# Kernel optimization log

Measured on AMD Instinct MI355X. Metric: run time of the kernel, lower is better.

Reference implementation:

```python
import jax, jax.numpy as jnp
import numpy as np

EPS = 1e-7  # Keras K.epsilon()


def setup_inputs() -> dict:
    key = jax.random.key(0)
    ks = jax.random.split(key, 8)
    B, T, D = 64, 2048, 256
    context = jax.random.normal(ks[0], (B, T, D), dtype=jnp.float32)
    aspect = jax.random.normal(ks[1], (B, D), dtype=jnp.float32)
    sentence = jax.random.normal(ks[2], (B, D), dtype=jnp.float32)
    context_mask = jax.random.randint(ks[3], (B, T), 0, 2).astype(bool)
    context_w = jax.random.normal(ks[4], (D, D), dtype=jnp.float32) * 0.05
    aspect_w = jax.random.normal(ks[5], (D, D), dtype=jnp.float32) * 0.05
    sent_w = jax.random.normal(ks[6], (D, D), dtype=jnp.float32) * 0.05
    attend_w = jax.random.normal(ks[7], (D, 1), dtype=jnp.float32) * 0.05
    return {"context": context, "aspect": aspect, "sentence": sentence,
            "context_mask": context_mask, "context_w": context_w,
            "aspect_w": aspect_w, "sent_w": sent_w, "attend_w": attend_w}


def reference(context, aspect, sentence, context_mask, context_w, aspect_w, sent_w, attend_w):
    # bias term from aspect/sentence, broadcast over time instead of K.repeat: [B,1,D]
    bias = (aspect @ aspect_w + sentence @ sent_w)[:, None, :]
    h = jnp.tanh(jnp.einsum('btd,de->bte', context, context_w) + bias)  # [B,T,D]
    g = jnp.einsum('btd,d->bt', h, attend_w[:, 0])                      # [B,T]
    a = jnp.exp(g) * context_mask.astype(jnp.float32)                   # faithful: no max-subtract
    a = a / (jnp.sum(a, axis=-1, keepdims=True) + EPS)
    attend_context = jnp.einsum('btd,bt->bd', context, a) + sentence     # [B,D]
    return attend_context
```

## Files before the change

### kernel.cpp

```cpp
#include <hip/hip_runtime.h>
#include <hip/hip_bf16.h>

#define BB  64
#define TT  2048
#define DD  256
#define EPSV 1e-7f
#define TILE_R 32
#define NTILE  8
#define NBLK   512

typedef __attribute__((ext_vector_type(8))) short bf16x8;
typedef __attribute__((ext_vector_type(4))) float f32x4;

__device__ __forceinline__ ushort f2bf(float f) {
    union { float f; unsigned u; } v; v.f = f;
    unsigned u = v.u;
    unsigned r = (u + 0x7FFFu + ((u >> 16) & 1u)) >> 16;
    return (ushort)r;
}

__device__ __forceinline__ float bf2f(unsigned h16) {
    union { unsigned u; float f; } v; v.u = h16 << 16;
    return v.f;
}

__device__ __forceinline__ unsigned pkbf(float lo, float hi) {
    union { float f; unsigned u; } a, b;
    a.f = lo; b.f = hi;
    return __builtin_amdgcn_perm(b.u + 0x8000u, a.u + 0x8000u, 0x07060302u);
}

__device__ __forceinline__ float tanh_fast(float x) {
    float e = __expf(2.0f * x);
    return 1.0f - 2.0f * __builtin_amdgcn_rcpf(e + 1.0f);
}

template<int CTRL>
__device__ __forceinline__ float dpp_rot_add(float x) {
    union { float f; int i; } a; a.f = x;
    int r = __builtin_amdgcn_update_dpp(0, a.i, CTRL, 0xF, 0xF, true);
    union { int i; float f; } b; b.i = r;
    return x + b.f;
}
__device__ __forceinline__ float row16_sum(float x) {
    x = dpp_rot_add<0x121>(x);
    x = dpp_rot_add<0x122>(x);
    x = dpp_rot_add<0x124>(x);
    x = dpp_rot_add<0x128>(x);
    return x;
}

__global__ __launch_bounds__(256) void prep_kernel(
    const float* __restrict__ aspect, const float* __restrict__ sentence,
    const float* __restrict__ context_w, const float* __restrict__ aspect_w,
    const float* __restrict__ sent_w,
    float* __restrict__ bias_part, ushort* __restrict__ wfrag_ws)
{
    const int blk = blockIdx.x, tid = threadIdx.x;
    if (blk < 512) {
        const int b = blk >> 3, q = blk & 7, e = tid;
        float s = 0.f;
        #pragma unroll 4
        for (int dd = 0; dd < 32; ++dd) {
            const int d = q * 32 + dd;
            s = fmaf(aspect[b * DD + d],   aspect_w[d * DD + e], s);
            s = fmaf(sentence[b * DD + d], sent_w[d * DD + e],   s);
        }
        bias_part[blk * DD + e] = s;
    } else {
        const int flat = (blk - 512) * 256 + tid;
        const int lane = flat & 63;
        const int kn   = flat >> 6;
        const int kk   = kn >> 4;
        const int n    = kn & 15;
        const int krow = kk * 32 + ((lane >> 4) << 3);
        const int col  = n * 16 + (lane & 15);
        bf16x8 v;
        #pragma unroll
        for (int j = 0; j < 8; ++j)
            v[j] = (short)f2bf(context_w[(size_t)(krow + j) * DD + col]);
        *reinterpret_cast<bf16x8*>(wfrag_ws + (size_t)flat * 8) = v;
    }
}

__global__ __launch_bounds__(512, 2) void attn_main(
    const float* __restrict__ ctx, const int* __restrict__ mask,
    const float* __restrict__ attend_w,
    const float* __restrict__ bias_part, const ushort* __restrict__ wfrag_ws,
    float* __restrict__ partial_ws, float* __restrict__ esum_ws)
{
    __shared__ __align__(16) char bfb[3][TILE_R * 512];
    __shared__ float gpartT[2][8][TILE_R];
    __shared__ float bias_lds[256];
    __shared__ float aw_lds[256];
    __shared__ float mask_lds[256];
    __shared__ float part_d[8][256];

    const int tid  = threadIdx.x;
    const int wave = tid >> 6;
    const int lane = tid & 63;
    const int blk  = blockIdx.x;
    const int b    = blk >> 3;
    const int cg   = wave;

    if (tid < 256) {
        float bs = 0.f;
        #pragma unroll
        for (int q = 0; q < 8; ++q) bs += bias_part[(b * 8 + q) * DD + tid];
        bias_lds[tid] = bs;
    } else {
        const int m = tid - 256;
        aw_lds[m]   = attend_w[m];
        mask_lds[m] = (float)mask[blk * 256 + m];
    }

    bf16x8 Bf[8][2];
    {
        const bf16x8* wf = reinterpret_cast<const bf16x8*>(wfrag_ws);
        #pragma unroll
        for (int kk = 0; kk < 8; ++kk) {
            Bf[kk][0] = wf[(kk * 16 + cg * 2 + 0) * 64 + lane];
            Bf[kk][1] = wf[(kk * 16 + cg * 2 + 1) * 64 + lane];
        }
    }

    const float4* src = reinterpret_cast<const float4*>(ctx);
    const int cc  = tid;
    const int crow0 = cc >> 5,        c80 = cc & 31;
    const int crow1 = (512 + cc) >> 5, c81 = (512 + cc) & 31;

    float4 sreg[4];
    {
        const size_t base4 = (size_t)(blk * NTILE) * 2048;
        #pragma unroll
        for (int i = 0; i < 2; ++i) {
            const int c = i * 512 + tid;
            sreg[2 * i + 0] = src[base4 + 2 * c + 0];
            sreg[2 * i + 1] = src[base4 + 2 * c + 1];
        }
        char* dst = bfb[0];
        #pragma unroll
        for (int i = 0; i < 2; ++i) {
            const int row = i ? crow1 : crow0, c8 = i ? c81 : c80;
            uint4 u;
            u.x = pkbf(sreg[2 * i].x,     sreg[2 * i].y);
            u.y = pkbf(sreg[2 * i].z,     sreg[2 * i].w);
            u.z = pkbf(sreg[2 * i + 1].x, sreg[2 * i + 1].y);
            u.w = pkbf(sreg[2 * i + 1].z, sreg[2 * i + 1].w);
            *reinterpret_cast<uint4*>(dst + row * 512 + ((c8 * 16) ^ ((row & 7) << 4))) = u;
        }
        const size_t b1 = base4 + 2048;
        #pragma unroll
        for (int i = 0; i < 2; ++i) {
            const int c = i * 512 + tid;
            sreg[2 * i + 0] = src[b1 + 2 * c + 0];
            sreg[2 * i + 1] = src[b1 + 2 * c + 1];
        }
    }
    __syncthreads();

    const int c0 = cg * 32 + (lane & 15), c1 = c0 + 16;
    const float bs0 = bias_lds[c0], awc0 = aw_lds[c0];
    const float bs1 = bias_lds[c1], awc1 = aw_lds[c1];

    float accd[4] = {0.f, 0.f, 0.f, 0.f};
    float es_acc = 0.f;
    int cb = 0;

    for (int it = 0; it < NTILE; ++it) {
        const int nb = (cb == 2) ? 0 : cb + 1;
        const int gp = it & 1;
        const char* lb = bfb[cb];

        if (it + 1 < NTILE) {
            char* dst = bfb[nb];
            #pragma unroll
            for (int i = 0; i < 2; ++i) {
                const int row = i ? crow1 : crow0, c8 = i ? c81 : c80;
                uint4 u;
                u.x = pkbf(sreg[2 * i].x,     sreg[2 * i].y);
                u.y = pkbf(sreg[2 * i].z,     sreg[2 * i].w);
                u.z = pkbf(sreg[2 * i + 1].x, sreg[2 * i + 1].y);
                u.w = pkbf(sreg[2 * i + 1].z, sreg[2 * i + 1].w);
                *reinterpret_cast<uint4*>(dst + row * 512 + ((c8 * 16) ^ ((row & 7) << 4))) = u;
            }
        }
        if (it + 2 < NTILE) {
            const size_t base4 = (size_t)(blk * NTILE + it + 2) * 2048;
            #pragma unroll
            for (int i = 0; i < 2; ++i) {
                const int c = i * 512 + tid;
                sreg[2 * i + 0] = src[base4 + 2 * c + 0];
                sreg[2 * i + 1] = src[base4 + 2 * c + 1];
            }
        }

        f32x4 acc[2][2];
        #pragma unroll
        for (int rt = 0; rt < 2; ++rt) {
            acc[rt][0] = (f32x4){0.f, 0.f, 0.f, 0.f};
            acc[rt][1] = (f32x4){0.f, 0.f, 0.f, 0.f};
        }
        #pragma unroll
        for (int rt = 0; rt < 2; ++rt) {
            const int row = rt * 16 + (lane & 15);
            const char* ab = lb + row * 512;
            const int asw = (row & 7) << 4;
            #pragma unroll
            for (int kk = 0; kk < 8; ++kk) {
                const bf16x8 a = *reinterpret_cast<const bf16x8*>(
                    ab + ((kk * 64 + ((lane >> 4) << 4)) ^ asw));
                acc[rt][0] = __builtin_amdgcn_mfma_f32_16x16x32_bf16(a, Bf[kk][0], acc[rt][0], 0, 0, 0);
                acc[rt][1] = __builtin_amdgcn_mfma_f32_16x16x32_bf16(a, Bf[kk][1], acc[rt][1], 0, 0, 0);
            }
        }

        #pragma unroll
        for (int rt = 0; rt < 2; ++rt) {
            float g0 = row16_sum(tanh_fast(acc[rt][0][0] + bs0) * awc0
                               + tanh_fast(acc[rt][1][0] + bs1) * awc1);
            float g1 = row16_sum(tanh_fast(acc[rt][0][1] + bs0) * awc0
                               + tanh_fast(acc[rt][1][1] + bs1) * awc1);
            float g2 = row16_sum(tanh_fast(acc[rt][0][2] + bs0) * awc0
                               + tanh_fast(acc[rt][1][2] + bs1) * awc1);
            float g3 = row16_sum(tanh_fast(acc[rt][0][3] + bs0) * awc0
                               + tanh_fast(acc[rt][1][3] + bs1) * awc1);
            if ((lane & 15) == 0) {
                const int r = rt * 16 + ((lane >> 4) << 2);
                *reinterpret_cast<float4*>(&gpartT[gp][cg][r]) = (float4){g0, g1, g2, g3};
            }
        }
        __syncthreads();

        const int erow = lane & 31;
        float gsum = 0.f;
        #pragma unroll
        for (int c = 0; c < 8; ++c) gsum += gpartT[gp][c][erow];
        const float ev = __expf(gsum) * mask_lds[it * TILE_R + erow];
        es_acc += (lane < 32) ? ev : 0.f;

        #pragma unroll
        for (int rr = 0; rr < 4; ++rr) {
            const int r = wave * 4 + rr;
            const float e = __shfl(ev, r);
            const uint2 hv = *reinterpret_cast<const uint2*>(
                lb + r * 512 + ((lane * 8) ^ ((r & 7) << 4)));
            accd[0] = fmaf(bf2f(hv.x & 0xffffu), e, accd[0]);
            accd[1] = fmaf(bf2f(hv.x >> 16),     e, accd[1]);
            accd[2] = fmaf(bf2f(hv.y & 0xffffu), e, accd[2]);
            accd[3] = fmaf(bf2f(hv.y >> 16),     e, accd[3]);
        }

        cb = nb;
    }

    *reinterpret_cast<float4*>(&part_d[wave][lane * 4]) =
        (float4){accd[0], accd[1], accd[2], accd[3]};
    __syncthreads();
    if (tid < 256) {
        float s = 0.f;
        #pragma unroll
        for (int w = 0; w < 8; ++w) s += part_d[w][tid];
        partial_ws[blk * DD + tid] = s;
    }
    if (wave == 0) {
        float s = row16_sum(es_acc);
        s += __shfl_xor(s, 16);
        if (lane == 0) esum_ws[blk] = s;
    }
}

__global__ __launch_bounds__(256) void finalize_kernel(
    const float* __restrict__ sentence, const float* __restrict__ partial_ws,
    const float* __restrict__ esum_ws, float* __restrict__ out)
{
    const int b = blockIdx.x, d = threadIdx.x;
    float es = 0.f, s = 0.f;
    #pragma unroll
    for (int i = 0; i < 8; ++i) {
        es += esum_ws[b * 8 + i];
        s  += partial_ws[(size_t)(b * 8 + i) * DD + d];
    }
    out[b * DD + d] = s / (es + EPSV) + sentence[b * DD + d];
}

extern "C" void kernel_launch(void* const* d_in, const int* in_sizes, int n_in,
                              void* d_out, int out_size, void* d_ws, size_t ws_size,
                              hipStream_t stream)
{
    const float* ctx       = (const float*)d_in[0];
    const float* aspect    = (const float*)d_in[1];
    const float* sentence  = (const float*)d_in[2];
    const int*   mask      = (const int*)  d_in[3];
    const float* context_w = (const float*)d_in[4];
    const float* aspect_w  = (const float*)d_in[5];
    const float* sent_w    = (const float*)d_in[6];
    const float* attend_w  = (const float*)d_in[7];
    float* out = (float*)d_out;

    char* ws = (char*)d_ws;
    ushort* wfrag_ws   = (ushort*)(ws);
    float*  bias_part  = (float*) (ws + 131072);
    float*  esum_ws    = (float*) (ws + 131072 + 524288);
    float*  partial_ws = (float*) (ws + 131072 + 524288 + 2048);

    prep_kernel<<<544, 256, 0, stream>>>(aspect, sentence, context_w, aspect_w, sent_w,
                                         bias_part, wfrag_ws);
    attn_main<<<NBLK, 512, 0, stream>>>(ctx, mask, attend_w, bias_part, wfrag_ws,
                                        partial_ws, esum_ws);
    finalize_kernel<<<BB, 256, 0, stream>>>(sentence, partial_ws, esum_ws, out);
}
```

Baseline: 46.89 us.

## Fuse prep kernel into attention kernel; compute bias and weight fragments in-block

Removes the separate prep launch. Each attention block now converts its own context_w fragments to bf16 straight from global memory and computes the aspect/sentence bias as two half-sums in LDS. The goal is to drop a kernel launch and the workspace round trip, and to overlap the first context tile loads with this setup work. In exchange every block (512 of them) redoes the 256x256x2 bias matvec for its batch and the strided weight conversion, which adds redundant global reads and ALU work. Launch bounds are also raised to 4 blocks per CU, which may constrain registers.

```diff
diff --git a/kernel.cpp b/kernel.cpp
--- a/kernel.cpp
+++ b/kernel.cpp
@@ -50,48 +50,17 @@
     return x;
 }
 
-__global__ __launch_bounds__(256) void prep_kernel(
+__global__ __launch_bounds__(512, 4) void attn_main(
+    const float* __restrict__ ctx, const int* __restrict__ mask,
+    const float* __restrict__ attend_w,
     const float* __restrict__ aspect, const float* __restrict__ sentence,
     const float* __restrict__ context_w, const float* __restrict__ aspect_w,
     const float* __restrict__ sent_w,
-    float* __restrict__ bias_part, ushort* __restrict__ wfrag_ws)
-{
-    const int blk = blockIdx.x, tid = threadIdx.x;
-    if (blk < 512) {
-        const int b = blk >> 3, q = blk & 7, e = tid;
-        float s = 0.f;
-        #pragma unroll 4
-        for (int dd = 0; dd < 32; ++dd) {
-            const int d = q * 32 + dd;
-            s = fmaf(aspect[b * DD + d],   aspect_w[d * DD + e], s);
-            s = fmaf(sentence[b * DD + d], sent_w[d * DD + e],   s);
-        }
-        bias_part[blk * DD + e] = s;
-    } else {
-        const int flat = (blk - 512) * 256 + tid;
-        const int lane = flat & 63;
-        const int kn   = flat >> 6;
-        const int kk   = kn >> 4;
-        const int n    = kn & 15;
-        const int krow = kk * 32 + ((lane >> 4) << 3);
-        const int col  = n * 16 + (lane & 15);
-        bf16x8 v;
-        #pragma unroll
-        for (int j = 0; j < 8; ++j)
-            v[j] = (short)f2bf(context_w[(size_t)(krow + j) * DD + col]);
-        *reinterpret_cast<bf16x8*>(wfrag_ws + (size_t)flat * 8) = v;
-    }
-}
-
-__global__ __launch_bounds__(512, 2) void attn_main(
-    const float* __restrict__ ctx, const int* __restrict__ mask,
-    const float* __restrict__ attend_w,
-    const float* __restrict__ bias_part, const ushort* __restrict__ wfrag_ws,
     float* __restrict__ partial_ws, float* __restrict__ esum_ws)
 {
     __shared__ __align__(16) char bfb[3][TILE_R * 512];
     __shared__ float gpartT[2][8][TILE_R];
-    __shared__ float bias_lds[256];
+    __shared__ float bias_half[2][256];
     __shared__ float aw_lds[256];
     __shared__ float mask_lds[256];
     __shared__ float part_d[8][256];
@@ -102,31 +71,11 @@
     const int blk  = blockIdx.x;
     const int b    = blk >> 3;
     const int cg   = wave;
-
-    if (tid < 256) {
-        float bs = 0.f;
-        #pragma unroll
-        for (int q = 0; q < 8; ++q) bs += bias_part[(b * 8 + q) * DD + tid];
-        bias_lds[tid] = bs;
-    } else {
-        const int m = tid - 256;
-        aw_lds[m]   = attend_w[m];
-        mask_lds[m] = (float)mask[blk * 256 + m];
-    }
-
-    bf16x8 Bf[8][2];
-    {
-        const bf16x8* wf = reinterpret_cast<const bf16x8*>(wfrag_ws);
-        #pragma unroll
-        for (int kk = 0; kk < 8; ++kk) {
-            Bf[kk][0] = wf[(kk * 16 + cg * 2 + 0) * 64 + lane];
-            Bf[kk][1] = wf[(kk * 16 + cg * 2 + 1) * 64 + lane];
-        }
-    }
+    const int l15  = lane & 15, hi = lane >> 4;
 
     const float4* src = reinterpret_cast<const float4*>(ctx);
     const int cc  = tid;
-    const int crow0 = cc >> 5,        c80 = cc & 31;
+    const int crow0 = cc >> 5,         c80 = cc & 31;
     const int crow1 = (512 + cc) >> 5, c81 = (512 + cc) & 31;
 
     float4 sreg[4];
@@ -138,6 +87,44 @@
             sreg[2 * i + 0] = src[base4 + 2 * c + 0];
             sreg[2 * i + 1] = src[base4 + 2 * c + 1];
         }
+    }
+
+    bf16x8 Bf[8][2];
+    #pragma unroll
+    for (int kk = 0; kk < 8; ++kk) {
+        #pragma unroll
+        for (int n2 = 0; n2 < 2; ++n2) {
+            const int col  = (cg * 2 + n2) * 16 + l15;
+            const int krow = kk * 32 + hi * 8;
+            const float* wp = context_w + (size_t)krow * DD + col;
+            bf16x8 v;
+            #pragma unroll
+            for (int j = 0; j < 8; ++j)
+                v[j] = (short)f2bf(wp[j * DD]);
+            Bf[kk][n2] = v;
+        }
+    }
+
+    if (tid < 256) {
+        aw_lds[tid]   = attend_w[tid];
+        mask_lds[tid] = (float)mask[blk * 256 + tid];
+    }
+    {
+        const int e = tid & 255, h = tid >> 8;
+        const float* ap = aspect   + b * DD + h * 128;
+        const float* sp = sentence + b * DD + h * 128;
+        const float* awp = aspect_w + (size_t)(h * 128) * DD + e;
+        const float* swp = sent_w   + (size_t)(h * 128) * DD + e;
+        float bsum = 0.f;
+        #pragma unroll 4
+        for (int dd = 0; dd < 128; ++dd) {
+            bsum = fmaf(ap[dd], awp[(size_t)dd * DD], bsum);
+            bsum = fmaf(sp[dd], swp[(size_t)dd * DD], bsum);
+        }
+        bias_half[h][e] = bsum;
+    }
+
+    {
         char* dst = bfb[0];
         #pragma unroll
         for (int i = 0; i < 2; ++i) {
@@ -149,7 +136,7 @@
             u.w = pkbf(sreg[2 * i + 1].z, sreg[2 * i + 1].w);
             *reinterpret_cast<uint4*>(dst + row * 512 + ((c8 * 16) ^ ((row & 7) << 4))) = u;
         }
-        const size_t b1 = base4 + 2048;
+        const size_t b1 = (size_t)(blk * NTILE + 1) * 2048;
         #pragma unroll
         for (int i = 0; i < 2; ++i) {
             const int c = i * 512 + tid;
@@ -159,9 +146,9 @@
     }
     __syncthreads();
 
-    const int c0 = cg * 32 + (lane & 15), c1 = c0 + 16;
-    const float bs0 = bias_lds[c0], awc0 = aw_lds[c0];
-    const float bs1 = bias_lds[c1], awc1 = aw_lds[c1];
+    const int c0 = cg * 32 + l15, c1 = c0 + 16;
+    const float bs0 = bias_half[0][c0] + bias_half[1][c0], awc0 = aw_lds[c0];
+    const float bs1 = bias_half[0][c1] + bias_half[1][c1], awc1 = aw_lds[c1];
 
     float accd[4] = {0.f, 0.f, 0.f, 0.f};
     float es_acc = 0.f;
@@ -203,13 +190,13 @@
         }
         #pragma unroll
         for (int rt = 0; rt < 2; ++rt) {
-            const int row = rt * 16 + (lane & 15);
+            const int row = rt * 16 + l15;
             const char* ab = lb + row * 512;
             const int asw = (row & 7) << 4;
             #pragma unroll
             for (int kk = 0; kk < 8; ++kk) {
                 const bf16x8 a = *reinterpret_cast<const bf16x8*>(
-                    ab + ((kk * 64 + ((lane >> 4) << 4)) ^ asw));
+                    ab + ((kk * 64 + (hi << 4)) ^ asw));
                 acc[rt][0] = __builtin_amdgcn_mfma_f32_16x16x32_bf16(a, Bf[kk][0], acc[rt][0], 0, 0, 0);
                 acc[rt][1] = __builtin_amdgcn_mfma_f32_16x16x32_bf16(a, Bf[kk][1], acc[rt][1], 0, 0, 0);
             }
@@ -225,8 +212,8 @@
                                + tanh_fast(acc[rt][1][2] + bs1) * awc1);
             float g3 = row16_sum(tanh_fast(acc[rt][0][3] + bs0) * awc0
                                + tanh_fast(acc[rt][1][3] + bs1) * awc1);
-            if ((lane & 15) == 0) {
-                const int r = rt * 16 + ((lane >> 4) << 2);
+            if (l15 == 0) {
+                const int r = rt * 16 + (hi << 2);
                 *reinterpret_cast<float4*>(&gpartT[gp][cg][r]) = (float4){g0, g1, g2, g3};
             }
         }
@@ -299,14 +286,11 @@
     float* out = (float*)d_out;
 
     char* ws = (char*)d_ws;
-    ushort* wfrag_ws   = (ushort*)(ws);
-    float*  bias_part  = (float*) (ws + 131072);
-    float*  esum_ws    = (float*) (ws + 131072 + 524288);
-    float*  partial_ws = (float*) (ws + 131072 + 524288 + 2048);
-
-    prep_kernel<<<544, 256, 0, stream>>>(aspect, sentence, context_w, aspect_w, sent_w,
-                                         bias_part, wfrag_ws);
-    attn_main<<<NBLK, 512, 0, stream>>>(ctx, mask, attend_w, bias_part, wfrag_ws,
+    float* esum_ws    = (float*)(ws);
+    float* partial_ws = (float*)(ws + 2048);
+
+    attn_main<<<NBLK, 512, 0, stream>>>(ctx, mask, attend_w, aspect, sentence,
+                                        context_w, aspect_w, sent_w,
                                         partial_ws, esum_ws);
     finalize_kernel<<<BB, 256, 0, stream>>>(sentence, partial_ws, esum_ws, out);
 }
```

Result: slower. 158.1 us (+237.3%).

## Software-pipeline weighted-sum stage one tile behind MFMA and raise MFMA priority

Applied to the files above, without the earlier changes.

Moves the exp/mask/weighted context accumulation for tile t to the start of iteration t+1, so it runs alongside the next tile's staging and MFMA work instead of right after the barrier. The LDS ring buffer grows from 3 to 4 slots so the previous tile's bf16 data stays valid while it is read. s_setprio is raised around the MFMA loop to favour matrix issue across waves. The extra 16KB of LDS per block may reduce occupancy under the 2-blocks-per-CU launch bound.

```diff
diff --git a/kernel.cpp b/kernel.cpp
--- a/kernel.cpp
+++ b/kernel.cpp
@@ -89,7 +89,7 @@
     const float* __restrict__ bias_part, const ushort* __restrict__ wfrag_ws,
     float* __restrict__ partial_ws, float* __restrict__ esum_ws)
 {
-    __shared__ __align__(16) char bfb[3][TILE_R * 512];
+    __shared__ __align__(16) char bfb[4][TILE_R * 512];
     __shared__ float gpartT[2][8][TILE_R];
     __shared__ float bias_lds[256];
     __shared__ float aw_lds[256];
@@ -102,6 +102,7 @@
     const int blk  = blockIdx.x;
     const int b    = blk >> 3;
     const int cg   = wave;
+    const int l15  = lane & 15, hi = lane >> 4;
 
     if (tid < 256) {
         float bs = 0.f;
@@ -126,7 +127,7 @@
 
     const float4* src = reinterpret_cast<const float4*>(ctx);
     const int cc  = tid;
-    const int crow0 = cc >> 5,        c80 = cc & 31;
+    const int crow0 = cc >> 5,         c80 = cc & 31;
     const int crow1 = (512 + cc) >> 5, c81 = (512 + cc) & 31;
 
     float4 sreg[4];
@@ -149,7 +150,7 @@
             u.w = pkbf(sreg[2 * i + 1].z, sreg[2 * i + 1].w);
             *reinterpret_cast<uint4*>(dst + row * 512 + ((c8 * 16) ^ ((row & 7) << 4))) = u;
         }
-        const size_t b1 = base4 + 2048;
+        const size_t b1 = (size_t)(blk * NTILE + 1) * 2048;
         #pragma unroll
         for (int i = 0; i < 2; ++i) {
             const int c = i * 512 + tid;
@@ -159,21 +160,42 @@
     }
     __syncthreads();
 
-    const int c0 = cg * 32 + (lane & 15), c1 = c0 + 16;
+    const int c0 = cg * 32 + l15, c1 = c0 + 16;
     const float bs0 = bias_lds[c0], awc0 = aw_lds[c0];
     const float bs1 = bias_lds[c1], awc1 = aw_lds[c1];
 
     float accd[4] = {0.f, 0.f, 0.f, 0.f};
     float es_acc = 0.f;
-    int cb = 0;
+
+    auto do_wsum = [&](int t) {
+        const char* pb = bfb[t & 3];
+        const int gp = t & 1;
+        const int erow = lane & 31;
+        float gsum = 0.f;
+        #pragma unroll
+        for (int c = 0; c < 8; ++c) gsum += gpartT[gp][c][erow];
+        const float ev = __expf(gsum) * mask_lds[t * TILE_R + erow];
+        es_acc += (lane < 32) ? ev : 0.f;
+        #pragma unroll
+        for (int rr = 0; rr < 4; ++rr) {
+            const int r = wave * 4 + rr;
+            const float e = __shfl(ev, r);
+            const uint2 hv = *reinterpret_cast<const uint2*>(
+                pb + r * 512 + ((lane * 8) ^ ((r & 7) << 4)));
+            accd[0] = fmaf(bf2f(hv.x & 0xffffu), e, accd[0]);
+            accd[1] = fmaf(bf2f(hv.x >> 16),     e, accd[1]);
+            accd[2] = fmaf(bf2f(hv.y & 0xffffu), e, accd[2]);
+            accd[3] = fmaf(bf2f(hv.y >> 16),     e, accd[3]);
+        }
+    };
 
     for (int it = 0; it < NTILE; ++it) {
-        const int nb = (cb == 2) ? 0 : cb + 1;
-        const int gp = it & 1;
-        const char* lb = bfb[cb];
+        const char* lb = bfb[it & 3];
+
+        if (it > 0) do_wsum(it - 1);
 
         if (it + 1 < NTILE) {
-            char* dst = bfb[nb];
+            char* dst = bfb[(it + 1) & 3];
             #pragma unroll
             for (int i = 0; i < 2; ++i) {
                 const int row = i ? crow1 : crow0, c8 = i ? c81 : c80;
@@ -201,20 +223,23 @@
             acc[rt][0] = (f32x4){0.f, 0.f, 0.f, 0.f};
             acc[rt][1] = (f32x4){0.f, 0.f, 0.f, 0.f};
         }
+        __builtin_amdgcn_s_setprio(1);
         #pragma unroll
         for (int rt = 0; rt < 2; ++rt) {
-            const int row = rt * 16 + (lane & 15);
+            const int row = rt * 16 + l15;
             const char* ab = lb + row * 512;
             const int asw = (row & 7) << 4;
             #pragma unroll
             for (int kk = 0; kk < 8; ++kk) {
                 const bf16x8 a = *reinterpret_cast<const bf16x8*>(
-                    ab + ((kk * 64 + ((lane >> 4) << 4)) ^ asw));
+                    ab + ((kk * 64 + (hi << 4)) ^ asw));
                 acc[rt][0] = __builtin_amdgcn_mfma_f32_16x16x32_bf16(a, Bf[kk][0], acc[rt][0], 0, 0, 0);
                 acc[rt][1] = __builtin_amdgcn_mfma_f32_16x16x32_bf16(a, Bf[kk][1], acc[rt][1], 0, 0, 0);
             }
         }
-
+        __builtin_amdgcn_s_setprio(0);
+
+        const int gp = it & 1;
         #pragma unroll
         for (int rt = 0; rt < 2; ++rt) {
             float g0 = row16_sum(tanh_fast(acc[rt][0][0] + bs0) * awc0
@@ -225,34 +250,15 @@
                                + tanh_fast(acc[rt][1][2] + bs1) * awc1);
             float g3 = row16_sum(tanh_fast(acc[rt][0][3] + bs0) * awc0
                                + tanh_fast(acc[rt][1][3] + bs1) * awc1);
-            if ((lane & 15) == 0) {
-                const int r = rt * 16 + ((lane >> 4) << 2);
+            if (l15 == 0) {
+                const int r = rt * 16 + (hi << 2);
                 *reinterpret_cast<float4*>(&gpartT[gp][cg][r]) = (float4){g0, g1, g2, g3};
             }
         }
         __syncthreads();
-
-        const int erow = lane & 31;
-        float gsum = 0.f;
-        #pragma unroll
-        for (int c = 0; c < 8; ++c) gsum += gpartT[gp][c][erow];
-        const float ev = __expf(gsum) * mask_lds[it * TILE_R + erow];
-        es_acc += (lane < 32) ? ev : 0.f;
-
-        #pragma unroll
-        for (int rr = 0; rr < 4; ++rr) {
-            const int r = wave * 4 + rr;
-            const float e = __shfl(ev, r);
-            const uint2 hv = *reinterpret_cast<const uint2*>(
-                lb + r * 512 + ((lane * 8) ^ ((r & 7) << 4)));
-            accd[0] = fmaf(bf2f(hv.x & 0xffffu), e, accd[0]);
-            accd[1] = fmaf(bf2f(hv.x >> 16),     e, accd[1]);
-            accd[2] = fmaf(bf2f(hv.y & 0xffffu), e, accd[2]);
-            accd[3] = fmaf(bf2f(hv.y >> 16),     e, accd[3]);
-        }
-
-        cb = nb;
-    }
+    }
+
+    do_wsum(NTILE - 1);
 
     *reinterpret_cast<float4*>(&part_d[wave][lane * 4]) =
         (float4){accd[0], accd[1], accd[2], accd[3]};
```

Result: slower. 48.33 us (+3.1%).
